# Optimization experiments

Hardware: AMD Instinct MI355X
Metric: run time of the kernel (lower is better)

## Reference

```python
import jax, jax.numpy as jnp
import numpy as np

IN_FEATURES = 4096
OUT_FEATURES = 4096
M_TOKENS = 8192
WEIGHT_SCALE = 0.1
OUT_SCALE = 0.1


def setup_inputs() -> dict:
    key = jax.random.key(0)
    k_x, k_w = jax.random.split(key)
    # int8-valued activations and weights in [-128, 128), stored as int32 carriers
    x_q = jax.random.randint(k_x, (M_TOKENS, IN_FEATURES), 0, 256, dtype=jnp.int32) - 128
    weight_q = jax.random.randint(k_w, (OUT_FEATURES, IN_FEATURES), 0, 256, dtype=jnp.int32) - 128
    scale_x = jnp.float32(0.05)
    return {"x_q": x_q, "weight_q": weight_q, "scale_x": scale_x}


def reference(x_q, weight_q, scale_x):
    acc = jnp.einsum("mk,nk->mn", x_q.astype(jnp.int32), weight_q.astype(jnp.int32))
    # fused epilogue: rescale, round-to-nearest, saturate to int8
    scale = scale_x * jnp.float32(WEIGHT_SCALE) / jnp.float32(OUT_SCALE)
    y = acc.astype(jnp.float32) * scale
    y_q = jnp.clip(jnp.round(y), -128.0, 127.0).astype(jnp.int8)
    return (y_q, jnp.float32(OUT_SCALE))
```

## Files before the change

kernel.cpp:

```cpp
#include <hip/hip_runtime.h>
#include <stdint.h>

typedef int v4i __attribute__((ext_vector_type(4)));

#define M_TOK 8192
#define N_OUT 4096
#define K_IN  4096

__global__ __launch_bounds__(256) void pack_int32_to_int8(
    const int4* __restrict__ src, int* __restrict__ dst, int n4)
{
    int i = blockIdx.x * blockDim.x + threadIdx.x;
    if (i >= n4) return;
    int4 a = src[i];
    dst[i] = (a.x & 255) | ((a.y & 255) << 8) | ((a.z & 255) << 16) | ((a.w & 255) << 24);
}

__global__ __launch_bounds__(256) void gemm_i8_kernel(
    const char* __restrict__ A8,
    const char* __restrict__ B8,
    const float* __restrict__ scale_ptr,
    float* __restrict__ out)
{
    __shared__ alignas(16) char lA[128 * 64];
    __shared__ alignas(16) char lB[128 * 64];

    const int tid  = threadIdx.x;
    const int wave = tid >> 6;
    const int lane = tid & 63;

    const int bm = blockIdx.y * 128;
    const int bn = blockIdx.x * 128;

    const int wm = (wave >> 1) * 64;
    const int wn = (wave & 1) * 64;

    v4i acc[4][4];
#pragma unroll
    for (int i = 0; i < 4; ++i)
#pragma unroll
        for (int j = 0; j < 4; ++j)
            acc[i][j] = (v4i){0, 0, 0, 0};

    const int srow = lane >> 2;
    const int scol = (lane & 3) * 16;
    const int ca0  = wave * 2;

    const char* gA0 = A8 + (size_t)(bm + ca0 * 16 + srow) * K_IN + scol;
    const char* gA1 = A8 + (size_t)(bm + ca0 * 16 + 16 + srow) * K_IN + scol;
    const char* gB0 = B8 + (size_t)(bn + ca0 * 16 + srow) * K_IN + scol;
    const char* gB1 = B8 + (size_t)(bn + ca0 * 16 + 16 + srow) * K_IN + scol;

    char* lA0 = lA + ca0 * 1024;
    char* lA1 = lA + (ca0 + 1) * 1024;
    char* lB0 = lB + ca0 * 1024;
    char* lB1 = lB + (ca0 + 1) * 1024;

    const int fm    = lane & 15;
    const int fquad = (lane >> 4) * 16;

    for (int k0 = 0; k0 < K_IN; k0 += 64) {
        __builtin_amdgcn_global_load_lds(
            (const __attribute__((address_space(1))) void*)(gA0 + k0),
            (__attribute__((address_space(3))) void*)lA0, 16, 0, 0);
        __builtin_amdgcn_global_load_lds(
            (const __attribute__((address_space(1))) void*)(gA1 + k0),
            (__attribute__((address_space(3))) void*)lA1, 16, 0, 0);
        __builtin_amdgcn_global_load_lds(
            (const __attribute__((address_space(1))) void*)(gB0 + k0),
            (__attribute__((address_space(3))) void*)lB0, 16, 0, 0);
        __builtin_amdgcn_global_load_lds(
            (const __attribute__((address_space(1))) void*)(gB1 + k0),
            (__attribute__((address_space(3))) void*)lB1, 16, 0, 0);

        __syncthreads();

        v4i af[4], bf[4];
#pragma unroll
        for (int i = 0; i < 4; ++i)
            af[i] = *(const v4i*)(lA + (wm + i * 16 + fm) * 64 + fquad);
#pragma unroll
        for (int j = 0; j < 4; ++j)
            bf[j] = *(const v4i*)(lB + (wn + j * 16 + fm) * 64 + fquad);

#pragma unroll
        for (int i = 0; i < 4; ++i)
#pragma unroll
            for (int j = 0; j < 4; ++j)
                acc[i][j] = __builtin_amdgcn_mfma_i32_16x16x64_i8(
                    af[i], bf[j], acc[i][j], 0, 0, 0);

        __syncthreads();
    }

    const float s     = scale_ptr[0];
    const float scale = (s * 0.1f) / 0.1f;
    const int rowg = (lane >> 4) * 4;
    const int coll = lane & 15;

#pragma unroll
    for (int i = 0; i < 4; ++i) {
#pragma unroll
        for (int j = 0; j < 4; ++j) {
#pragma unroll
            for (int r = 0; r < 4; ++r) {
                int row = bm + wm + i * 16 + rowg + r;
                int col = bn + wn + j * 16 + coll;
                float y = (float)acc[i][j][r] * scale;
                y = rintf(y);
                y = fminf(fmaxf(y, -128.0f), 127.0f);
                out[(size_t)row * N_OUT + col] = y;
            }
        }
    }

    if (bm == 0 && bn == 0 && tid == 0)
        out[(size_t)M_TOK * N_OUT] = 0.1f;
}

extern "C" void kernel_launch(void* const* d_in, const int* in_sizes, int n_in,
                              void* d_out, int out_size, void* d_ws, size_t ws_size,
                              hipStream_t stream)
{
    const int*   x_q     = (const int*)d_in[0];
    const int*   w_q     = (const int*)d_in[1];
    const float* scale_x = (const float*)d_in[2];
    float* out = (float*)d_out;

    char* A8 = (char*)d_ws;
    char* B8 = (char*)d_ws + (size_t)M_TOK * K_IN;

    const int n4x = (M_TOK * K_IN) / 4;
    const int n4w = (N_OUT * K_IN) / 4;

    pack_int32_to_int8<<<n4x / 256, 256, 0, stream>>>(
        (const int4*)x_q, (int*)A8, n4x);
    pack_int32_to_int8<<<n4w / 256, 256, 0, stream>>>(
        (const int4*)w_q, (int*)B8, n4w);

    dim3 grid(N_OUT / 128, M_TOK / 128);
    gemm_i8_kernel<<<grid, 256, 0, stream>>>(A8, B8, scale_x, out);
}
```

Baseline: 416.8 us.

## Switch to 32x32x32 MFMA, K-tile 128 with XOR-swizzled LDS, fuse pack kernels

The GEMM main loop now stages 128-wide K tiles into shared memory with an XOR swizzle on the 16-byte column chunks, which should avoid LDS bank conflicts on fragment reads. It also moves from 16x16x64 to 32x32x32 int8 MFMA with a 2x2 set of 16-register accumulators per wave. Together these halve the number of barriers per K and cut the fragment loads per MFMA. The two int32-to-int8 pack launches are merged into one kernel to save a launch. The risks are higher register pressure and changed occupancy from the doubled LDS footprint.

After: 400.8 us. 3.9% less time.

```diff
diff --git a/kernel.cpp b/kernel.cpp
--- a/kernel.cpp
+++ b/kernel.cpp
@@ -1,19 +1,28 @@
 #include <hip/hip_runtime.h>
 #include <stdint.h>
 
-typedef int v4i __attribute__((ext_vector_type(4)));
+typedef int v4i  __attribute__((ext_vector_type(4)));
+typedef int v16i __attribute__((ext_vector_type(16)));
 
 #define M_TOK 8192
 #define N_OUT 4096
 #define K_IN  4096
 
-__global__ __launch_bounds__(256) void pack_int32_to_int8(
-    const int4* __restrict__ src, int* __restrict__ dst, int n4)
+__device__ __forceinline__ int pack4(int4 a) {
+    return (a.x & 255) | ((a.y & 255) << 8) | ((a.z & 255) << 16) | ((a.w & 255) << 24);
+}
+
+__global__ __launch_bounds__(256) void pack_both(
+    const int4* __restrict__ x, const int4* __restrict__ w,
+    int* __restrict__ dA, int* __restrict__ dB, int n4x, int n4w)
 {
     int i = blockIdx.x * blockDim.x + threadIdx.x;
-    if (i >= n4) return;
-    int4 a = src[i];
-    dst[i] = (a.x & 255) | ((a.y & 255) << 8) | ((a.z & 255) << 16) | ((a.w & 255) << 24);
+    if (i < n4x) {
+        dA[i] = pack4(x[i]);
+    } else {
+        int j = i - n4x;
+        if (j < n4w) dB[j] = pack4(w[j]);
+    }
 }
 
 __global__ __launch_bounds__(256) void gemm_i8_kernel(
@@ -22,8 +31,8 @@
     const float* __restrict__ scale_ptr,
     float* __restrict__ out)
 {
-    __shared__ alignas(16) char lA[128 * 64];
-    __shared__ alignas(16) char lB[128 * 64];
+    __shared__ alignas(16) char lA[128 * 128];
+    __shared__ alignas(16) char lB[128 * 128];
 
     const int tid  = threadIdx.x;
     const int wave = tid >> 6;
@@ -35,78 +44,78 @@
     const int wm = (wave >> 1) * 64;
     const int wn = (wave & 1) * 64;
 
-    v4i acc[4][4];
+    v16i acc[2][2];
 #pragma unroll
-    for (int i = 0; i < 4; ++i)
+    for (int i = 0; i < 2; ++i)
 #pragma unroll
-        for (int j = 0; j < 4; ++j)
-            acc[i][j] = (v4i){0, 0, 0, 0};
+        for (int j = 0; j < 2; ++j)
+#pragma unroll
+            for (int r = 0; r < 16; ++r)
+                acc[i][j][r] = 0;
 
-    const int srow = lane >> 2;
-    const int scol = (lane & 3) * 16;
-    const int ca0  = wave * 2;
+    const int srow = lane >> 3;
+    const int scol = ((lane & 7) ^ srow) << 4;
 
-    const char* gA0 = A8 + (size_t)(bm + ca0 * 16 + srow) * K_IN + scol;
-    const char* gA1 = A8 + (size_t)(bm + ca0 * 16 + 16 + srow) * K_IN + scol;
-    const char* gB0 = B8 + (size_t)(bn + ca0 * 16 + srow) * K_IN + scol;
-    const char* gB1 = B8 + (size_t)(bn + ca0 * 16 + 16 + srow) * K_IN + scol;
+    const char* gA[4]; const char* gB[4];
+    char* lAp[4]; char* lBp[4];
+#pragma unroll
+    for (int q = 0; q < 4; ++q) {
+        int row0 = wave * 32 + q * 8;
+        gA[q] = A8 + (size_t)(bm + row0 + srow) * K_IN + scol;
+        gB[q] = B8 + (size_t)(bn + row0 + srow) * K_IN + scol;
+        lAp[q] = lA + row0 * 128;
+        lBp[q] = lB + row0 * 128;
+    }
 
-    char* lA0 = lA + ca0 * 1024;
-    char* lA1 = lA + (ca0 + 1) * 1024;
-    char* lB0 = lB + ca0 * 1024;
-    char* lB1 = lB + (ca0 + 1) * 1024;
+    const int fm = lane & 31;
+    const int fh = lane >> 5;
+    const int fsw = fm & 7;
 
-    const int fm    = lane & 15;
-    const int fquad = (lane >> 4) * 16;
-
-    for (int k0 = 0; k0 < K_IN; k0 += 64) {
-        __builtin_amdgcn_global_load_lds(
-            (const __attribute__((address_space(1))) void*)(gA0 + k0),
-            (__attribute__((address_space(3))) void*)lA0, 16, 0, 0);
-        __builtin_amdgcn_global_load_lds(
-            (const __attribute__((address_space(1))) void*)(gA1 + k0),
-            (__attribute__((address_space(3))) void*)lA1, 16, 0, 0);
-        __builtin_amdgcn_global_load_lds(
-            (const __attribute__((address_space(1))) void*)(gB0 + k0),
-            (__attribute__((address_space(3))) void*)lB0, 16, 0, 0);
-        __builtin_amdgcn_global_load_lds(
-            (const __attribute__((address_space(1))) void*)(gB1 + k0),
-            (__attribute__((address_space(3))) void*)lB1, 16, 0, 0);
+    for (int k0 = 0; k0 < K_IN; k0 += 128) {
+#pragma unroll
+        for (int q = 0; q < 4; ++q) {
+            __builtin_amdgcn_global_load_lds(
+                (const __attribute__((address_space(1))) void*)(gA[q] + k0),
+                (__attribute__((address_space(3))) void*)lAp[q], 16, 0, 0);
+            __builtin_amdgcn_global_load_lds(
+                (const __attribute__((address_space(1))) void*)(gB[q] + k0),
+                (__attribute__((address_space(3))) void*)lBp[q], 16, 0, 0);
+        }
 
         __syncthreads();
 
-        v4i af[4], bf[4];
 #pragma unroll
-        for (int i = 0; i < 4; ++i)
-            af[i] = *(const v4i*)(lA + (wm + i * 16 + fm) * 64 + fquad);
+        for (int kk = 0; kk < 4; ++kk) {
+            const int goff = ((kk * 2 + fh) ^ fsw) << 4;
+            v4i af[2], bf[2];
 #pragma unroll
-        for (int j = 0; j < 4; ++j)
-            bf[j] = *(const v4i*)(lB + (wn + j * 16 + fm) * 64 + fquad);
-
+            for (int t = 0; t < 2; ++t) {
+                af[t] = *(const v4i*)(lA + (wm + t * 32 + fm) * 128 + goff);
+                bf[t] = *(const v4i*)(lB + (wn + t * 32 + fm) * 128 + goff);
+            }
 #pragma unroll
-        for (int i = 0; i < 4; ++i)
+            for (int ti = 0; ti < 2; ++ti)
 #pragma unroll
-            for (int j = 0; j < 4; ++j)
-                acc[i][j] = __builtin_amdgcn_mfma_i32_16x16x64_i8(
-                    af[i], bf[j], acc[i][j], 0, 0, 0);
+                for (int tj = 0; tj < 2; ++tj)
+                    acc[ti][tj] = __builtin_amdgcn_mfma_i32_32x32x32_i8(
+                        af[ti], bf[tj], acc[ti][tj], 0, 0, 0);
+        }
 
         __syncthreads();
     }
 
     const float s     = scale_ptr[0];
     const float scale = (s * 0.1f) / 0.1f;
-    const int rowg = (lane >> 4) * 4;
-    const int coll = lane & 15;
 
 #pragma unroll
-    for (int i = 0; i < 4; ++i) {
+    for (int ti = 0; ti < 2; ++ti) {
 #pragma unroll
-        for (int j = 0; j < 4; ++j) {
+        for (int tj = 0; tj < 2; ++tj) {
 #pragma unroll
-            for (int r = 0; r < 4; ++r) {
-                int row = bm + wm + i * 16 + rowg + r;
-                int col = bn + wn + j * 16 + coll;
-                float y = (float)acc[i][j][r] * scale;
+            for (int r = 0; r < 16; ++r) {
+                int row = bm + wm + ti * 32 + (r & 3) + 8 * (r >> 2) + 4 * fh;
+                int col = bn + wn + tj * 32 + fm;
+                float y = (float)acc[ti][tj][r] * scale;
                 y = rintf(y);
                 y = fminf(fmaxf(y, -128.0f), 127.0f);
                 out[(size_t)row * N_OUT + col] = y;
@@ -133,10 +142,8 @@
     const int n4x = (M_TOK * K_IN) / 4;
     const int n4w = (N_OUT * K_IN) / 4;
 
-    pack_int32_to_int8<<<n4x / 256, 256, 0, stream>>>(
-        (const int4*)x_q, (int*)A8, n4x);
-    pack_int32_to_int8<<<n4w / 256, 256, 0, stream>>>(
-        (const int4*)w_q, (int*)B8, n4w);
+    pack_both<<<(n4x + n4w) / 256, 256, 0, stream>>>(
+        (const int4*)x_q, (const int4*)w_q, (int*)A8, (int*)B8, n4x, n4w);
 
     dim3 grid(N_OUT / 128, M_TOK / 128);
     gemm_i8_kernel<<<grid, 256, 0, stream>>>(A8, B8, scale_x, out);
```
